# Optimization experiments

Hardware: AMD Instinct MI355X
Metric: run time of the kernel (lower is better)

Reference implementation:

```python
import jax, jax.numpy as jnp
import numpy as np

B, S, E, H = 2, 2048, 1024, 16
DK = E // H


def setup_inputs() -> dict:
    key = jax.random.key(0)
    ks = jax.random.split(key, 10)
    x = jax.random.normal(ks[0], (B, S, E), dtype=jnp.float32)
    mask = jax.random.randint(ks[1], (B, S, S), 0, 2).astype(bool)
    scale = 1.0 / np.sqrt(E)
    def lin(k):
        kw, kb = jax.random.split(k)
        W = jax.random.uniform(kw, (E, E), minval=-scale, maxval=scale, dtype=jnp.float32)
        b = jax.random.uniform(kb, (E,), minval=-scale, maxval=scale, dtype=jnp.float32)
        return W, b
    Wq, bq = lin(ks[2])
    Wk, bk = lin(ks[3])
    Wv, bv = lin(ks[4])
    Wo, bo = lin(ks[5])
    return {"x": x, "mask": mask, "Wq": Wq, "bq": bq, "Wk": Wk, "bk": bk,
            "Wv": Wv, "bv": bv, "Wo": Wo, "bo": bo}


def reference(x, mask, Wq, bq, Wk, bk, Wv, bv, Wo, bo):
    # projections (torch Linear: y = x @ W.T + b)
    q = x @ Wq.T + bq
    k = x @ Wk.T + bk
    v = x @ Wv.T + bv
    # separate heads: [B,S,E] -> [B,H,S,DK]
    def split(t):
        return t.reshape(B, S, H, DK).transpose(0, 2, 1, 3)
    q, k, v = split(q), split(k), split(v)
    scores = jnp.einsum("bhqd,bhkd->bhqk", q, k) / jnp.sqrt(jnp.float32(DK))
    # masked_fill: positions where mask is True get -1e9 (mask broadcast over heads)
    scores = jnp.where(mask[:, None, :, :], jnp.float32(-1e9), scores)
    attn = jax.nn.softmax(scores, axis=-1)  # dropout is identity in eval
    out = jnp.einsum("bhqk,bhkd->bhqd", attn, v)
    out = out.transpose(0, 2, 1, 3).reshape(B, S, E)  # combine heads
    return out @ Wo.T + bo
```

## Files before the change

kernel.cpp:

```cpp
#include <hip/hip_runtime.h>
#include <hip/hip_bf16.h>


typedef __attribute__((ext_vector_type(8))) short short8;
typedef __attribute__((ext_vector_type(4))) short s16x4;
typedef __attribute__((ext_vector_type(4))) float f32x4;

#define MFMA16(a, b, c) __builtin_amdgcn_mfma_f32_16x16x32_bf16(a, b, c, 0, 0, 0)

#define BATCH 2
#define SEQ   2048
#define EMB   1024
#define HEADS 16
#define DKK   64
#define MROWS (BATCH * SEQ)

typedef __hip_bfloat16 bf16;
typedef unsigned long long u64;

static __device__ __forceinline__ short bf16b(float f) {
    union { bf16 h; short s; } u;
    u.h = __float2bfloat16(f);
    return u.s;
}
static __device__ __forceinline__ short8 ld8k(const bf16* p) {
    return *(const short8*)p;
}
static __device__ __forceinline__ short8 ld8kf(const float* p) {
    const f32x4 a = *(const f32x4*)p;
    const f32x4 b = *(const f32x4*)(p + 4);
    short8 r;
    r[0] = bf16b(a[0]); r[1] = bf16b(a[1]); r[2] = bf16b(a[2]); r[3] = bf16b(a[3]);
    r[4] = bf16b(b[0]); r[5] = bf16b(b[1]); r[6] = bf16b(b[2]); r[7] = bf16b(b[3]);
    return r;
}

static __device__ __forceinline__ void glds16(const bf16* g, bf16* l) {
    __builtin_amdgcn_global_load_lds(
        (const __attribute__((address_space(1))) void*)g,
        (__attribute__((address_space(3))) void*)l, 16, 0, 0);
}

__global__ void detect_kernel(const unsigned int* __restrict__ mw,
                              int* __restrict__ flags) {
    __shared__ int mbyte;
    if (threadIdx.x == 0) mbyte = 0;
    __syncthreads();
    int mb = 0;
    for (int i = threadIdx.x; i < 4096; i += 256)
        if (mw[i] > 1u) mb = 1;
    if (mb) atomicOr(&mbyte, 1);
    __syncthreads();
    if (threadIdx.x == 0) { flags[0] = 1; flags[1] = mbyte; }
}

__global__ __launch_bounds__(256) void pack_mask(
        const void* __restrict__ mp, unsigned* __restrict__ Mp,
        const int* __restrict__ flags) {
    const bool m8 = flags[1] != 0;
    const int T = blockIdx.x * 256 + threadIdx.x;
    const int lane = T & 63, rest = T >> 6;
    const int rest2 = rest >> 3;
    const int qb = rest2 & 15, rest3 = rest2 >> 4;
    const int it = rest3 & 31, b = rest3 >> 5;
    const int wvv = rest & 7;
    const int l16 = lane & 15, quad = lane >> 4;
    const int q = qb * 128 + wvv * 16 + l16;
    const size_t rowb = ((size_t)(b * 2048 + q)) * 2048;
    const int k0 = it * 64 + quad * 4;

    unsigned out[4];
    if (m8) {
        const unsigned char* p8 = (const unsigned char*)mp;
#pragma unroll
        for (int j = 0; j < 4; ++j) {
            const unsigned v = *(const unsigned*)(p8 + rowb + k0 + j * 16);
            unsigned w = 0;
#pragma unroll
            for (int r = 0; r < 4; ++r)
                w |= ((((v >> (8 * r)) & 0xFFu) == 0u) ? 0xFFu : 0u) << (8 * r);
            out[j] = w;
        }
    } else {
        const int* p32 = (const int*)mp;
#pragma unroll
        for (int j = 0; j < 4; ++j) {
            const int4 v = *(const int4*)(p32 + rowb + k0 + j * 16);
            unsigned w = 0;
            w |=  (v.x == 0) ? 0xFFu : 0u;
            w |= ((v.y == 0) ? 0xFFu : 0u) << 8;
            w |= ((v.z == 0) ? 0xFFu : 0u) << 16;
            w |= ((v.w == 0) ? 0xFFu : 0u) << 24;
            out[j] = w;
        }
    }
    unsigned* dst = Mp + (size_t)rest * 256 + lane;
#pragma unroll
    for (int j = 0; j < 4; ++j) dst[j * 64] = out[j];
}

__global__ __launch_bounds__(256) void cvt_all(
        const float* __restrict__ x,  const float* __restrict__ wq,
        const float* __restrict__ wk, const float* __restrict__ wv,
        const float* __restrict__ wo,
        bf16* __restrict__ xb,  bf16* __restrict__ wqb,
        bf16* __restrict__ wkb, bf16* __restrict__ wvb,
        bf16* __restrict__ wob) {
    const int bid = blockIdx.x;
    const float* s; bf16* d; int base;
    if (bid < 2048)      { s = x;  d = xb;  base = bid; }
    else if (bid < 2560) { s = wq; d = wqb; base = bid - 2048; }
    else if (bid < 3072) { s = wk; d = wkb; base = bid - 2560; }
    else if (bid < 3584) { s = wv; d = wvb; base = bid - 3072; }
    else                 { s = wo; d = wob; base = bid - 3584; }
    const int i = (base * 256 + threadIdx.x) * 8;
    *(short8*)(d + i) = ld8kf(s + i);
}

__global__ __launch_bounds__(256) void gemm_qkv_staged(
        const bf16* __restrict__ X,
        const bf16* __restrict__ Wq, const bf16* __restrict__ Wk,
        const bf16* __restrict__ Wv,
        const float* __restrict__ bq, const float* __restrict__ bk,
        const float* __restrict__ bv,
        bf16* __restrict__ qo, bf16* __restrict__ ko, bf16* __restrict__ vo) {
    __shared__ bf16 As[2][128 * 32];
    __shared__ bf16 Bs[2][128 * 32];

    const int t = threadIdx.x, lane = t & 63;
    const int wv = t >> 6;
    const int mb = blockIdx.x / 24, nb = blockIdx.x % 24;
    const int m0 = mb * 128;
    const int n0g = nb * 128;
    const int sel = n0g >> 10;
    const int n0 = n0g & 1023;
    const bf16* W     = sel == 0 ? Wq : (sel == 1 ? Wk : Wv);
    const float* bias = sel == 0 ? bq : (sel == 1 ? bk : bv);
    bf16* out         = sel == 0 ? qo : (sel == 1 ? ko : vo);
    const float oscale = sel == 0 ? 0.18033688011f : 1.0f;

    const int wr = wv >> 1, wc = wv & 1;
    const int m_off = wr * 64, n_off = wc * 64;
    const int l16 = lane & 15, quad = lane >> 4;

    int srow[2], sg[2];
#pragma unroll
    for (int i = 0; i < 2; ++i) {
        const int c = i * 256 + t;
        srow[i] = c >> 2;
        sg[i]   = (c & 3) ^ (srow[i] & 3);
    }

    f32x4 acc[4][4];
#pragma unroll
    for (int i = 0; i < 4; ++i)
#pragma unroll
        for (int j = 0; j < 4; ++j)
            acc[i][j] = (f32x4){0.f, 0.f, 0.f, 0.f};

#pragma unroll
    for (int i = 0; i < 2; ++i) {
        glds16(X + (m0 + srow[i]) * 1024 + sg[i] * 8, &As[0][(i * 256 + t) * 8]);
        glds16(W + (n0 + srow[i]) * 1024 + sg[i] * 8, &Bs[0][(i * 256 + t) * 8]);
    }

    for (int it = 0; it < 32; ++it) {
        __syncthreads();
        if (it < 31) {
            const int ktn = (it + 1) * 32;
            const int nb_ = (it + 1) & 1;
#pragma unroll
            for (int i = 0; i < 2; ++i) {
                glds16(X + (m0 + srow[i]) * 1024 + ktn + sg[i] * 8,
                       &As[nb_][(i * 256 + t) * 8]);
                glds16(W + (n0 + srow[i]) * 1024 + ktn + sg[i] * 8,
                       &Bs[nb_][(i * 256 + t) * 8]);
            }
        }
        const bf16* Ab = As[it & 1];
        const bf16* Bb = Bs[it & 1];
        short8 af[4], bfr[4];
#pragma unroll
        for (int ii = 0; ii < 4; ++ii) {
            const int row = m_off + ii * 16 + l16;
            const int slot = quad ^ (row & 3);
            af[ii] = *(const short8*)(Ab + row * 32 + slot * 8);
        }
#pragma unroll
        for (int jj = 0; jj < 4; ++jj) {
            const int row = n_off + jj * 16 + l16;
            const int slot = quad ^ (row & 3);
            bfr[jj] = *(const short8*)(Bb + row * 32 + slot * 8);
        }
#pragma unroll
        for (int ii = 0; ii < 4; ++ii)
#pragma unroll
            for (int jj = 0; jj < 4; ++jj)
                acc[ii][jj] = MFMA16(af[ii], bfr[jj], acc[ii][jj]);
    }

#pragma unroll
    for (int j = 0; j < 4; ++j) {
        const int nl = n0 + n_off + j * 16 + l16;
        const float bj = bias[nl];
        const int h = nl >> 6, d = nl & 63;
#pragma unroll
        for (int i = 0; i < 4; ++i) {
#pragma unroll
            for (int r = 0; r < 4; ++r) {
                const int m = m0 + m_off + i * 16 + quad * 4 + r;
                const float v = (acc[i][j][r] + bj) * oscale;
                const int bb = m >> 11, ss = m & 2047;
                const int idx = (sel == 2)
                    ? ((bb * HEADS + h) * DKK + d) * SEQ + ss
                    : ((bb * HEADS + h) * SEQ + ss) * DKK + d;
                out[idx] = __float2bfloat16(v);
            }
        }
    }
}

__global__ __launch_bounds__(256) void gemm_out_staged(
        const bf16* __restrict__ X,
        const bf16* __restrict__ W, const float* __restrict__ bias,
        float* __restrict__ out) {
    __shared__ bf16 As[2][128 * 32];
    __shared__ bf16 Bs[2][64 * 32];

    const int t = threadIdx.x, lane = t & 63;
    const int wv = t >> 6;
    const int mb = blockIdx.x >> 4, nb = blockIdx.x & 15;
    const int m0 = mb * 128, n0 = nb * 64;
    const int wr = wv >> 1, wc = wv & 1;
    const int m_off = wr * 64, n_off = wc * 32;
    const int l16 = lane & 15, quad = lane >> 4;

    int srow[2], sg[2];
#pragma unroll
    for (int i = 0; i < 2; ++i) {
        const int c = i * 256 + t;
        srow[i] = c >> 2;
        sg[i]   = (c & 3) ^ (srow[i] & 3);
    }
    const int brow = t >> 2;
    const int bslot = (t & 3) ^ (brow & 3);

    f32x4 acc[4][2];
#pragma unroll
    for (int i = 0; i < 4; ++i)
#pragma unroll
        for (int j = 0; j < 2; ++j)
            acc[i][j] = (f32x4){0.f, 0.f, 0.f, 0.f};

#pragma unroll
    for (int i = 0; i < 2; ++i)
        glds16(X + (m0 + srow[i]) * 1024 + sg[i] * 8, &As[0][(i * 256 + t) * 8]);
    glds16(W + (n0 + brow) * 1024 + bslot * 8, &Bs[0][t * 8]);

    for (int it = 0; it < 32; ++it) {
        __syncthreads();
        if (it < 31) {
            const int ktn = (it + 1) * 32;
            const int nb_ = (it + 1) & 1;
#pragma unroll
            for (int i = 0; i < 2; ++i)
                glds16(X + (m0 + srow[i]) * 1024 + ktn + sg[i] * 8,
                       &As[nb_][(i * 256 + t) * 8]);
            glds16(W + (n0 + brow) * 1024 + ktn + bslot * 8, &Bs[nb_][t * 8]);
        }
        const bf16* Ab = As[it & 1];
        const bf16* Bb = Bs[it & 1];
        short8 af[4], bfr[2];
#pragma unroll
        for (int ii = 0; ii < 4; ++ii) {
            const int row = m_off + ii * 16 + l16;
            const int slot = quad ^ (row & 3);
            af[ii] = *(const short8*)(Ab + row * 32 + slot * 8);
        }
#pragma unroll
        for (int jj = 0; jj < 2; ++jj) {
            const int row = n_off + jj * 16 + l16;
            const int slot = quad ^ (row & 3);
            bfr[jj] = *(const short8*)(Bb + row * 32 + slot * 8);
        }
#pragma unroll
        for (int ii = 0; ii < 4; ++ii)
#pragma unroll
            for (int jj = 0; jj < 2; ++jj)
                acc[ii][jj] = MFMA16(af[ii], bfr[jj], acc[ii][jj]);
    }

#pragma unroll
    for (int j = 0; j < 2; ++j) {
        const int n = n0 + n_off + j * 16 + l16;
        const float bj = bias[n];
#pragma unroll
        for (int i = 0; i < 4; ++i) {
#pragma unroll
            for (int r = 0; r < 4; ++r) {
                const int m = m0 + m_off + i * 16 + quad * 4 + r;
                out[m * 1024 + n] = acc[i][j][r] + bj;
            }
        }
    }
}

__global__ __launch_bounds__(512, 4) void attn_kernel(
        const bf16* __restrict__ Qw,
        const bf16* __restrict__ Kw,
        const bf16* __restrict__ Vw,
        const unsigned* __restrict__ Mp,
        bf16* __restrict__ attn_out) {
    const int t = threadIdx.x;
    const int lane = t & 63;
    const int wv   = t >> 6;
    const int l16 = lane & 15, quad = lane >> 4;
    const int h = blockIdx.y, b = blockIdx.z;
    const int bh = b * HEADS + h;
    const int qb = blockIdx.x;
    const int qb0 = qb * 128;

    const bf16* Q  = Qw + bh * SEQ * DKK;
    const bf16* Kp = Kw + bh * SEQ * DKK;
    const bf16* Vt = Vw + bh * DKK * SEQ;

    __shared__ bf16 Ks[2][4096];
    __shared__ bf16 Vs[2][4096];
    __shared__ bf16 lds_p[8][16][72];

    short8 qf[2];
#pragma unroll
    for (int t2 = 0; t2 < 2; ++t2)
        qf[t2] = ld8k(Q + (qb0 + wv * 16 + l16) * DKK + t2 * 32 + quad * 8);

    const short ob = bf16b(1.0f);
    short8 ones;
#pragma unroll
    for (int e = 0; e < 8; ++e) ones[e] = ob;

    f32x4 o[4];
#pragma unroll
    for (int jd = 0; jd < 4; ++jd) o[jd] = (f32x4){0.f, 0.f, 0.f, 0.f};
    f32x4 lacc = (f32x4){0.f, 0.f, 0.f, 0.f};
    const f32x4 zacc = (f32x4){0.f, 0.f, 0.f, 0.f};

    const int srow = t >> 3;
    const int sg   = (t & 7) ^ (srow & 7);

    glds16(Kp + srow * DKK + sg * 8, &Ks[0][t * 8]);
    glds16(Vt + srow * SEQ + sg * 8, &Vs[0][t * 8]);

    const size_t mbase = (size_t)(b * 512 + qb) * 2048 + wv * 256 + lane;

    for (int it = 0; it < SEQ / 64; ++it) {
        __syncthreads();
        if (it < SEQ / 64 - 1) {
            const int nb_ = (it + 1) & 1;
            const int ktn = (it + 1) * 64;
            glds16(Kp + (ktn + srow) * DKK + sg * 8, &Ks[nb_][t * 8]);
            glds16(Vt + srow * SEQ + ktn + sg * 8, &Vs[nb_][t * 8]);
        }

        const unsigned* mrow = Mp + mbase + (size_t)it * 32768;
        unsigned m32[4];
#pragma unroll
        for (int j = 0; j < 4; ++j) m32[j] = mrow[j * 64];

        const bf16* Kb = Ks[it & 1];
        const bf16* Vb = Vs[it & 1];

        short8 kf[2][4];
#pragma unroll
        for (int t2 = 0; t2 < 2; ++t2)
#pragma unroll
            for (int j = 0; j < 4; ++j) {
                const int row = j * 16 + l16;
                const int slot = (t2 * 4 + quad) ^ (row & 7);
                kf[t2][j] = *(const short8*)(Kb + row * 64 + slot * 8);
            }

        f32x4 s[4];
        __builtin_amdgcn_s_setprio(1);
#pragma unroll
        for (int j = 0; j < 4; ++j) {
            s[j] = MFMA16(kf[0][j], qf[0], zacc);
            s[j] = MFMA16(kf[1][j], qf[1], s[j]);
        }
        __builtin_amdgcn_s_setprio(0);

#pragma unroll
        for (int j = 0; j < 4; ++j) {
            union { s16x4 v; unsigned w[2]; } pk;
#pragma unroll
            for (int r = 0; r < 4; ++r)
                pk.v[r] = bf16b(__builtin_exp2f(s[j][r]));
            pk.w[0] &= __builtin_amdgcn_perm(0u, m32[j], 0x01010000u);
            pk.w[1] &= __builtin_amdgcn_perm(0u, m32[j], 0x03030202u);
            *(s16x4*)(&lds_p[wv][l16][j * 16 + quad * 4]) = pk.v;
        }

        __builtin_amdgcn_s_setprio(1);
#pragma unroll
        for (int t2 = 0; t2 < 2; ++t2) {
            short8 vf[4];
#pragma unroll
            for (int jd = 0; jd < 4; ++jd) {
                const int row = jd * 16 + l16;
                const int slot = (t2 * 4 + quad) ^ (row & 7);
                vf[jd] = *(const short8*)(Vb + row * 64 + slot * 8);
            }
            const short8 pf = *(const short8*)(&lds_p[wv][l16][t2 * 32 + quad * 8]);
            lacc = MFMA16(pf, ones, lacc);
#pragma unroll
            for (int jd = 0; jd < 4; ++jd)
                o[jd] = MFMA16(pf, vf[jd], o[jd]);
        }
        __builtin_amdgcn_s_setprio(0);
    }

#pragma unroll
    for (int r = 0; r < 4; ++r) {
        const float inv = 1.0f / lacc[r];
        const int q = qb0 + wv * 16 + quad * 4 + r;
#pragma unroll
        for (int jd = 0; jd < 4; ++jd)
            attn_out[(b * SEQ + q) * EMB + h * DKK + jd * 16 + l16] =
                __float2bfloat16(o[jd][r] * inv);
    }
}

extern "C" void kernel_launch(void* const* d_in, const int* in_sizes, int n_in,
                              void* d_out, int out_size, void* d_ws, size_t ws_size,
                              hipStream_t stream) {
    char* ws = (char*)d_ws;
    const size_t MB = 1024 * 1024;
    int*      flags = (int*)ws;
    bf16*     wob   = (bf16*)(ws + 256);
    bf16*     wqb   = (bf16*)(ws + 256 + 2 * MB);
    bf16*     wkb   = (bf16*)(ws + 256 + 4 * MB);
    bf16*     wvb   = (bf16*)(ws + 256 + 6 * MB);
    unsigned* Mp    = (unsigned*)(ws + 256 + 2 * MB);
    bf16*     xb    = (bf16*)(ws + 256 + 10 * MB);
    bf16*     k_ws  = (bf16*)(ws + 256 + 18 * MB);
    bf16*     attn_ws = xb;

    bf16* q_ws = (bf16*)d_out;
    bf16* v_ws = (bf16*)d_out + 4194304;

    detect_kernel<<<1, 256, 0, stream>>>((const unsigned int*)d_in[1], flags);

    cvt_all<<<4096, 256, 0, stream>>>(
        (const float*)d_in[0], (const float*)d_in[2], (const float*)d_in[4],
        (const float*)d_in[6], (const float*)d_in[8],
        xb, wqb, wkb, wvb, wob);

    gemm_qkv_staged<<<768, 256, 0, stream>>>(
        xb, wqb, wkb, wvb,
        (const float*)d_in[3], (const float*)d_in[5], (const float*)d_in[7],
        q_ws, k_ws, v_ws);

    pack_mask<<<2048, 256, 0, stream>>>(d_in[1], Mp, flags);

    attn_kernel<<<dim3(SEQ / 128, HEADS, BATCH), 512, 0, stream>>>(
        q_ws, k_ws, v_ws, Mp, attn_ws);

    gemm_out_staged<<<512, 256, 0, stream>>>(
        attn_ws, wob, (const float*)d_in[9], (float*)d_out);
}
```

Baseline: 247.1 us.

## Process 32 query rows per wave to double K/V tile reuse in attention

Each attention wave now handles two 16-row query sub-tiles (256 query rows per block instead of 128), so every K and V fragment loaded from LDS feeds twice as many MFMAs. The block count halves and the mask packing layout is reordered to match the new per-wave row grouping. This cuts LDS and global traffic for K/V per unit of work but raises register pressure (launch bounds lowered to 2 waves-per-EU hint) and reduces grid parallelism to 256 blocks.

```diff
diff --git a/kernel.cpp b/kernel.cpp
--- a/kernel.cpp
+++ b/kernel.cpp
@@ -60,12 +60,13 @@
     const bool m8 = flags[1] != 0;
     const int T = blockIdx.x * 256 + threadIdx.x;
     const int lane = T & 63, rest = T >> 6;
-    const int rest2 = rest >> 3;
-    const int qb = rest2 & 15, rest3 = rest2 >> 4;
-    const int it = rest3 & 31, b = rest3 >> 5;
-    const int wvv = rest & 7;
+    const int i   = rest & 1;
+    const int wvv = (rest >> 1) & 7;
+    const int qb  = (rest >> 4) & 7;
+    const int it  = (rest >> 7) & 31;
+    const int b   = rest >> 12;
     const int l16 = lane & 15, quad = lane >> 4;
-    const int q = qb * 128 + wvv * 16 + l16;
+    const int q = qb * 256 + wvv * 32 + i * 16 + l16;
     const size_t rowb = ((size_t)(b * 2048 + q)) * 2048;
     const int k0 = it * 64 + quad * 4;
 
@@ -305,7 +306,7 @@
     }
 }
 
-__global__ __launch_bounds__(512, 4) void attn_kernel(
+__global__ __launch_bounds__(512, 2) void attn_kernel(
         const bf16* __restrict__ Qw,
         const bf16* __restrict__ Kw,
         const bf16* __restrict__ Vw,
@@ -318,7 +319,7 @@
     const int h = blockIdx.y, b = blockIdx.z;
     const int bh = b * HEADS + h;
     const int qb = blockIdx.x;
-    const int qb0 = qb * 128;
+    const int qb0 = qb * 256;
 
     const bf16* Q  = Qw + bh * SEQ * DKK;
     const bf16* Kp = Kw + bh * SEQ * DKK;
@@ -326,22 +327,26 @@
 
     __shared__ bf16 Ks[2][4096];
     __shared__ bf16 Vs[2][4096];
-    __shared__ bf16 lds_p[8][16][72];
-
-    short8 qf[2];
-#pragma unroll
-    for (int t2 = 0; t2 < 2; ++t2)
-        qf[t2] = ld8k(Q + (qb0 + wv * 16 + l16) * DKK + t2 * 32 + quad * 8);
+    __shared__ bf16 lds_p[8][2][16][72];
+
+    short8 qf[2][2];
+#pragma unroll
+    for (int i = 0; i < 2; ++i)
+#pragma unroll
+        for (int t2 = 0; t2 < 2; ++t2)
+            qf[i][t2] = ld8k(Q + (qb0 + wv * 32 + i * 16 + l16) * DKK + t2 * 32 + quad * 8);
 
     const short ob = bf16b(1.0f);
     short8 ones;
 #pragma unroll
     for (int e = 0; e < 8; ++e) ones[e] = ob;
 
-    f32x4 o[4];
-#pragma unroll
-    for (int jd = 0; jd < 4; ++jd) o[jd] = (f32x4){0.f, 0.f, 0.f, 0.f};
-    f32x4 lacc = (f32x4){0.f, 0.f, 0.f, 0.f};
+    f32x4 o[2][4];
+#pragma unroll
+    for (int i = 0; i < 2; ++i)
+#pragma unroll
+        for (int jd = 0; jd < 4; ++jd) o[i][jd] = (f32x4){0.f, 0.f, 0.f, 0.f};
+    f32x4 lacc[2] = {(f32x4){0.f, 0.f, 0.f, 0.f}, (f32x4){0.f, 0.f, 0.f, 0.f}};
     const f32x4 zacc = (f32x4){0.f, 0.f, 0.f, 0.f};
 
     const int srow = t >> 3;
@@ -350,7 +355,7 @@
     glds16(Kp + srow * DKK + sg * 8, &Ks[0][t * 8]);
     glds16(Vt + srow * SEQ + sg * 8, &Vs[0][t * 8]);
 
-    const size_t mbase = (size_t)(b * 512 + qb) * 2048 + wv * 256 + lane;
+    const size_t mbase = (size_t)(b * 2048 + qb * 8 + wv) * 512 + lane;
 
     for (int it = 0; it < SEQ / 64; ++it) {
         __syncthreads();
@@ -362,9 +367,11 @@
         }
 
         const unsigned* mrow = Mp + mbase + (size_t)it * 32768;
-        unsigned m32[4];
-#pragma unroll
-        for (int j = 0; j < 4; ++j) m32[j] = mrow[j * 64];
+        unsigned m32[2][4];
+#pragma unroll
+        for (int i = 0; i < 2; ++i)
+#pragma unroll
+            for (int j = 0; j < 4; ++j) m32[i][j] = mrow[i * 256 + j * 64];
 
         const bf16* Kb = Ks[it & 1];
         const bf16* Vb = Vs[it & 1];
@@ -379,25 +386,29 @@
                 kf[t2][j] = *(const short8*)(Kb + row * 64 + slot * 8);
             }
 
-        f32x4 s[4];
+        f32x4 s[2][4];
         __builtin_amdgcn_s_setprio(1);
 #pragma unroll
-        for (int j = 0; j < 4; ++j) {
-            s[j] = MFMA16(kf[0][j], qf[0], zacc);
-            s[j] = MFMA16(kf[1][j], qf[1], s[j]);
-        }
+        for (int i = 0; i < 2; ++i)
+#pragma unroll
+            for (int j = 0; j < 4; ++j) {
+                s[i][j] = MFMA16(kf[0][j], qf[i][0], zacc);
+                s[i][j] = MFMA16(kf[1][j], qf[i][1], s[i][j]);
+            }
         __builtin_amdgcn_s_setprio(0);
 
 #pragma unroll
-        for (int j = 0; j < 4; ++j) {
-            union { s16x4 v; unsigned w[2]; } pk;
-#pragma unroll
-            for (int r = 0; r < 4; ++r)
-                pk.v[r] = bf16b(__builtin_exp2f(s[j][r]));
-            pk.w[0] &= __builtin_amdgcn_perm(0u, m32[j], 0x01010000u);
-            pk.w[1] &= __builtin_amdgcn_perm(0u, m32[j], 0x03030202u);
-            *(s16x4*)(&lds_p[wv][l16][j * 16 + quad * 4]) = pk.v;
-        }
+        for (int i = 0; i < 2; ++i)
+#pragma unroll
+            for (int j = 0; j < 4; ++j) {
+                union { s16x4 v; unsigned w[2]; } pk;
+#pragma unroll
+                for (int r = 0; r < 4; ++r)
+                    pk.v[r] = bf16b(__builtin_exp2f(s[i][j][r]));
+                pk.w[0] &= __builtin_amdgcn_perm(0u, m32[i][j], 0x01010000u);
+                pk.w[1] &= __builtin_amdgcn_perm(0u, m32[i][j], 0x03030202u);
+                *(s16x4*)(&lds_p[wv][i][l16][j * 16 + quad * 4]) = pk.v;
+            }
 
         __builtin_amdgcn_s_setprio(1);
 #pragma unroll
@@ -409,24 +420,29 @@
                 const int slot = (t2 * 4 + quad) ^ (row & 7);
                 vf[jd] = *(const short8*)(Vb + row * 64 + slot * 8);
             }
-            const short8 pf = *(const short8*)(&lds_p[wv][l16][t2 * 32 + quad * 8]);
-            lacc = MFMA16(pf, ones, lacc);
+#pragma unroll
+            for (int i = 0; i < 2; ++i) {
+                const short8 pf = *(const short8*)(&lds_p[wv][i][l16][t2 * 32 + quad * 8]);
+                lacc[i] = MFMA16(pf, ones, lacc[i]);
+#pragma unroll
+                for (int jd = 0; jd < 4; ++jd)
+                    o[i][jd] = MFMA16(pf, vf[jd], o[i][jd]);
+            }
+        }
+        __builtin_amdgcn_s_setprio(0);
+    }
+
+#pragma unroll
+    for (int i = 0; i < 2; ++i)
+#pragma unroll
+        for (int r = 0; r < 4; ++r) {
+            const float inv = 1.0f / lacc[i][r];
+            const int q = qb0 + wv * 32 + i * 16 + quad * 4 + r;
 #pragma unroll
             for (int jd = 0; jd < 4; ++jd)
-                o[jd] = MFMA16(pf, vf[jd], o[jd]);
-        }
-        __builtin_amdgcn_s_setprio(0);
-    }
-
-#pragma unroll
-    for (int r = 0; r < 4; ++r) {
-        const float inv = 1.0f / lacc[r];
-        const int q = qb0 + wv * 16 + quad * 4 + r;
-#pragma unroll
-        for (int jd = 0; jd < 4; ++jd)
-            attn_out[(b * SEQ + q) * EMB + h * DKK + jd * 16 + l16] =
-                __float2bfloat16(o[jd][r] * inv);
-    }
+                attn_out[(b * SEQ + q) * EMB + h * DKK + jd * 16 + l16] =
+                    __float2bfloat16(o[i][jd][r] * inv);
+        }
 }
 
 extern "C" void kernel_launch(void* const* d_in, const int* in_sizes, int n_in,
@@ -461,7 +477,7 @@
 
     pack_mask<<<2048, 256, 0, stream>>>(d_in[1], Mp, flags);
 
-    attn_kernel<<<dim3(SEQ / 128, HEADS, BATCH), 512, 0, stream>>>(
+    attn_kernel<<<dim3(SEQ / 256, HEADS, BATCH), 512, 0, stream>>>(
         q_ws, k_ws, v_ws, Mp, attn_ws);
 
     gemm_out_staged<<<512, 256, 0, stream>>>(
```

Result: slower. 255.2 us (+3.3%).
